# Performance work log

Measured on AMD Instinct MI355X. Metric: run time of the kernel, lower is better.

## Reference

```python
import jax, jax.numpy as jnp
import numpy as np

B, S, D, H, DK, DV, DFF, WIN = 2, 2048, 1024, 16, 64, 64, 4096, 128


def _layernorm(x, g, b, eps=1e-5):
    m = jnp.mean(x, axis=-1, keepdims=True)
    v = jnp.var(x, axis=-1, keepdims=True)
    return (x - m) / jnp.sqrt(v + eps) * g + b


def _attn_block(x, wq, bq, wk, bk, wv, bv, wo, bo, g, be, use_band):
    bsz, seq = x.shape[0], x.shape[1]
    q = (x @ wq + bq).reshape(bsz, seq, H, DK).transpose(0, 2, 1, 3)  # [B,H,S,DK]
    k = (x @ wk + bk).reshape(bsz, seq, H, DK).transpose(0, 2, 1, 3)
    v = (x @ wv + bv).reshape(bsz, seq, H, DV).transpose(0, 2, 1, 3)
    scores = jnp.einsum('bhqd,bhkd->bhqk', q, k) / np.sqrt(DK).astype(x.dtype)
    if use_band:
        i = jnp.arange(seq)
        band = jnp.abs(i[:, None] - i[None, :]) < WIN  # |i-j| < n_window
        scores = jnp.where(band[None, None], scores, -jnp.inf)
    attn = jax.nn.softmax(scores, axis=-1)
    ctx = jnp.einsum('bhqk,bhkd->bhqd', attn, v)  # [B,H,S,DV]
    ctx = ctx.transpose(0, 2, 1, 3).reshape(bsz, seq, H * DV)
    out = ctx @ wo + bo
    return _layernorm(out + x, g, be), attn


def _ffn(x, wc1, bc1, wc2, bc2, g, be):
    # conv1d with kernel_size=1 == pointwise linear
    h = jax.nn.relu(x @ wc1 + bc1)
    out = h @ wc2 + bc2
    return _layernorm(out + x, g, be)


def setup_inputs() -> dict:
    key = jax.random.key(0)
    ks = jax.random.split(key, 16)
    sc = 0.02
    inp = {'x': jax.random.normal(ks[0], (B, S, D), jnp.float32)}
    def lin(k, i, o):
        return jax.random.normal(k, (i, o), jnp.float32) * sc
    # full MHA params
    inp.update(wq1=lin(ks[1], D, H * DK), bq1=jnp.zeros((H * DK,)),
               wk1=lin(ks[2], D, H * DK), bk1=jnp.zeros((H * DK,)),
               wv1=lin(ks[3], D, H * DV), bv1=jnp.zeros((H * DV,)),
               wo1=lin(ks[4], H * DV, D), bo1=jnp.zeros((D,)),
               g1=jnp.ones((D,)), be1=jnp.zeros((D,)))
    # sliding-window attention params
    inp.update(wq2=lin(ks[5], D, H * DK), bq2=jnp.zeros((H * DK,)),
               wk2=lin(ks[6], D, H * DK), bk2=jnp.zeros((H * DK,)),
               wv2=lin(ks[7], D, H * DV), bv2=jnp.zeros((H * DV,)),
               wo2=lin(ks[8], H * DV, D), bo2=jnp.zeros((D,)),
               g2=jnp.ones((D,)), be2=jnp.zeros((D,)))
    # FFN params (conv1d k=1 -> linear)
    inp.update(wc1=lin(ks[9], D, DFF), bc1=jnp.zeros((DFF,)),
               wc2=lin(ks[10], DFF, D), bc2=jnp.zeros((D,)),
               g3=jnp.ones((D,)), be3=jnp.zeros((D,)))
    return inp


def reference(x, wq1, bq1, wk1, bk1, wv1, bv1, wo1, bo1, g1, be1,
              wq2, bq2, wk2, bk2, wv2, bv2, wo2, bo2, g2, be2,
              wc1, bc1, wc2, bc2, g3, be3):
    full_out, attn = _attn_block(x, wq1, bq1, wk1, bk1, wv1, bv1, wo1, bo1, g1, be1, use_band=False)
    sw_out, _ = _attn_block(x, wq2, bq2, wk2, bk2, wv2, bv2, wo2, bo2, g2, be2, use_band=True)
    enc = _ffn(full_out + sw_out, wc1, bc1, wc2, bc2, g3, be3)
    return enc, attn
```

## Files before the change

kernel.cpp:

```cpp
#include <hip/hip_runtime.h>
#include <hip/hip_bf16.h>

typedef __bf16 bf16_t;
typedef bf16_t bf16x8 __attribute__((ext_vector_type(8)));
typedef float floatx4 __attribute__((ext_vector_type(4)));

#define BBS 2
#define SEQ 2048
#define DIM 1024
#define NH 16
#define HD 64
#define DFF_ 4096
#define NT (BBS*SEQ)

template<bool AF32, bool BF32, bool BT, bool OUTF32, bool RELU, bool BIAS>
__global__ __launch_bounds__(256) void gemm64(
    const void* __restrict__ Av, const void* __restrict__ Bv,
    const float* __restrict__ bias, void* __restrict__ Cout,
    int M, int N, int K, int lda, int ldb, int ldc,
    int batchH, long long sAb, long long sAh, long long sBb, long long sBh,
    long long sCb, long long sCh, float scale)
{
    int z = blockIdx.z;
    int zb = z / batchH, zh = z - zb * batchH;
    long long aoff = zb * sAb + zh * sAh;
    long long boff = zb * sBb + zh * sBh;
    long long coff = zb * sCb + zh * sCh;
    const bf16_t* A16 = (const bf16_t*)Av + aoff;
    const float*  A32 = (const float*)Av + aoff;
    const bf16_t* B16 = (const bf16_t*)Bv + boff;
    const float*  B32 = (const float*)Bv + boff;

    int tile_n = blockIdx.x * 64;
    int tile_m = blockIdx.y * 64;

    __shared__ __align__(16) bf16_t Alds[64 * 72];
    __shared__ __align__(16) bf16_t Blds[64 * 72];

    int tid  = threadIdx.x;
    int wave = tid >> 6;
    int lane = tid & 63;
    int lm = lane & 15;
    int lq = lane >> 4;

    floatx4 acc[4];
    #pragma unroll
    for (int i = 0; i < 4; ++i) acc[i] = (floatx4){0.f, 0.f, 0.f, 0.f};

    int s_row  = tid >> 2;
    int s_koff = (tid & 3) * 16;
    int nb_k   = tid >> 3;
    int nb_noff= (tid & 7) * 8;

    int nkt = K >> 6;
    for (int kt = 0; kt < nkt; ++kt) {
        int k0 = kt << 6;
        if constexpr (AF32) {
            const float* src = A32 + (long long)(tile_m + s_row) * lda + (k0 + s_koff);
            float4 f0 = ((const float4*)src)[0];
            float4 f1 = ((const float4*)src)[1];
            float4 f2 = ((const float4*)src)[2];
            float4 f3 = ((const float4*)src)[3];
            bf16x8 h0, h1;
            h0[0]=(bf16_t)f0.x; h0[1]=(bf16_t)f0.y; h0[2]=(bf16_t)f0.z; h0[3]=(bf16_t)f0.w;
            h0[4]=(bf16_t)f1.x; h0[5]=(bf16_t)f1.y; h0[6]=(bf16_t)f1.z; h0[7]=(bf16_t)f1.w;
            h1[0]=(bf16_t)f2.x; h1[1]=(bf16_t)f2.y; h1[2]=(bf16_t)f2.z; h1[3]=(bf16_t)f2.w;
            h1[4]=(bf16_t)f3.x; h1[5]=(bf16_t)f3.y; h1[6]=(bf16_t)f3.z; h1[7]=(bf16_t)f3.w;
            *(bf16x8*)&Alds[s_row * 72 + s_koff]     = h0;
            *(bf16x8*)&Alds[s_row * 72 + s_koff + 8] = h1;
        } else {
            const bf16_t* src = A16 + (long long)(tile_m + s_row) * lda + (k0 + s_koff);
            *(uint4*)&Alds[s_row * 72 + s_koff]     = *(const uint4*)src;
            *(uint4*)&Alds[s_row * 72 + s_koff + 8] = *(const uint4*)(src + 8);
        }
        if constexpr (BT) {
            const bf16_t* src = B16 + (long long)(tile_n + s_row) * ldb + (k0 + s_koff);
            *(uint4*)&Blds[s_row * 72 + s_koff]     = *(const uint4*)src;
            *(uint4*)&Blds[s_row * 72 + s_koff + 8] = *(const uint4*)(src + 8);
        } else if constexpr (BF32) {
            #pragma unroll
            for (int kk = 0; kk < 64; kk += 32) {
                int k = kk + nb_k;
                const float* src = B32 + (long long)(k0 + k) * ldb + (tile_n + nb_noff);
                float4 f0 = ((const float4*)src)[0];
                float4 f1 = ((const float4*)src)[1];
                Blds[(nb_noff + 0) * 72 + k] = (bf16_t)f0.x;
                Blds[(nb_noff + 1) * 72 + k] = (bf16_t)f0.y;
                Blds[(nb_noff + 2) * 72 + k] = (bf16_t)f0.z;
                Blds[(nb_noff + 3) * 72 + k] = (bf16_t)f0.w;
                Blds[(nb_noff + 4) * 72 + k] = (bf16_t)f1.x;
                Blds[(nb_noff + 5) * 72 + k] = (bf16_t)f1.y;
                Blds[(nb_noff + 6) * 72 + k] = (bf16_t)f1.z;
                Blds[(nb_noff + 7) * 72 + k] = (bf16_t)f1.w;
            }
        } else {
            #pragma unroll
            for (int kk = 0; kk < 64; kk += 32) {
                int k = kk + nb_k;
                bf16x8 v = *(const bf16x8*)(B16 + (long long)(k0 + k) * ldb + (tile_n + nb_noff));
                #pragma unroll
                for (int j = 0; j < 8; ++j)
                    Blds[(nb_noff + j) * 72 + k] = v[j];
            }
        }
        __syncthreads();
        #pragma unroll
        for (int ks = 0; ks < 2; ++ks) {
            bf16x8 af = *(const bf16x8*)&Alds[(wave * 16 + lm) * 72 + ks * 32 + lq * 8];
            #pragma unroll
            for (int nt = 0; nt < 4; ++nt) {
                bf16x8 bfr = *(const bf16x8*)&Blds[(nt * 16 + lm) * 72 + ks * 32 + lq * 8];
                acc[nt] = __builtin_amdgcn_mfma_f32_16x16x32_bf16(af, bfr, acc[nt], 0, 0, 0);
            }
        }
        __syncthreads();
    }

    #pragma unroll
    for (int nt = 0; nt < 4; ++nt) {
        int col = tile_n + nt * 16 + lm;
        float bv = 0.f;
        if constexpr (BIAS) bv = bias[col];
        #pragma unroll
        for (int r = 0; r < 4; ++r) {
            int row = tile_m + wave * 16 + lq * 4 + r;
            float v = acc[nt][r] * scale + bv;
            if constexpr (RELU) v = fmaxf(v, 0.f);
            long long idx = coff + (long long)row * ldc + col;
            if constexpr (OUTF32) ((float*)Cout)[idx] = v;
            else                  ((bf16_t*)Cout)[idx] = (bf16_t)v;
        }
    }
}

__global__ __launch_bounds__(256) void softmax_f32(float* __restrict__ p)
{
    int row  = blockIdx.x * 4 + (threadIdx.x >> 6);
    int lane = threadIdx.x & 63;
    float* pr = p + (long long)row * SEQ;
    float v[32];
    float mx = -3.4e38f;
    #pragma unroll
    for (int it = 0; it < 8; ++it) {
        float4 c = *(const float4*)(pr + it * 256 + lane * 4);
        v[it*4+0] = c.x; v[it*4+1] = c.y; v[it*4+2] = c.z; v[it*4+3] = c.w;
        mx = fmaxf(mx, fmaxf(fmaxf(c.x, c.y), fmaxf(c.z, c.w)));
    }
    for (int off = 32; off; off >>= 1) mx = fmaxf(mx, __shfl_xor(mx, off));
    float s = 0.f;
    #pragma unroll
    for (int i = 0; i < 32; ++i) { v[i] = __expf(v[i] - mx); s += v[i]; }
    for (int off = 32; off; off >>= 1) s += __shfl_xor(s, off);
    float inv = 1.f / s;
    #pragma unroll
    for (int it = 0; it < 8; ++it) {
        float4 c;
        c.x = v[it*4+0]*inv; c.y = v[it*4+1]*inv; c.z = v[it*4+2]*inv; c.w = v[it*4+3]*inv;
        *(float4*)(pr + it * 256 + lane * 4) = c;
    }
}

__global__ __launch_bounds__(256) void sw_attn_mfma(
    const bf16_t* __restrict__ Q, const bf16_t* __restrict__ K,
    const bf16_t* __restrict__ V, bf16_t* __restrict__ ctx)
{
    int qt = blockIdx.x, h = blockIdx.y, b = blockIdx.z;
    int i0 = qt * 64;
    long long headoff = (long long)b * SEQ * DIM + (long long)h * HD;
    const bf16_t* Qb = Q + headoff;
    const bf16_t* Kb = K + headoff;
    const bf16_t* Vb = V + headoff;

    __shared__ __align__(16) bf16_t Klds[64 * 72];
    __shared__ __align__(16) bf16_t Vlds[64 * 72];
    __shared__ __align__(16) bf16_t Plds[64 * 72];

    int tid  = threadIdx.x;
    int wave = tid >> 6;
    int lane = tid & 63;
    int lm = lane & 15;
    int lq = lane >> 4;
    int s_row  = tid >> 2;
    int s_koff = (tid & 3) * 16;
    int nb_j   = tid >> 3;
    int nb_doff= (tid & 7) * 8;

    {
        const bf16_t* src = Qb + (long long)(i0 + s_row) * DIM + s_koff;
        *(uint4*)&Klds[s_row * 72 + s_koff]     = *(const uint4*)src;
        *(uint4*)&Klds[s_row * 72 + s_koff + 8] = *(const uint4*)(src + 8);
    }
    __syncthreads();
    bf16x8 qf0 = *(const bf16x8*)&Klds[(wave * 16 + lm) * 72 + 0 * 32 + lq * 8];
    bf16x8 qf1 = *(const bf16x8*)&Klds[(wave * 16 + lm) * 72 + 1 * 32 + lq * 8];
    __syncthreads();

    float m[4], l[4];
    floatx4 oacc[4];
    #pragma unroll
    for (int r = 0; r < 4; ++r) { m[r] = -1e30f; l[r] = 0.f; }
    #pragma unroll
    for (int nt = 0; nt < 4; ++nt) oacc[nt] = (floatx4){0.f, 0.f, 0.f, 0.f};

    int ibase = i0 + wave * 16 + lq * 4;

    for (int t = 0; t < 5; ++t) {
        int j0 = i0 - 128 + t * 64;
        if (j0 < 0 || j0 >= SEQ) continue;
        {
            const bf16_t* src = Kb + (long long)(j0 + s_row) * DIM + s_koff;
            *(uint4*)&Klds[s_row * 72 + s_koff]     = *(const uint4*)src;
            *(uint4*)&Klds[s_row * 72 + s_koff + 8] = *(const uint4*)(src + 8);
        }
        #pragma unroll
        for (int jj = 0; jj < 64; jj += 32) {
            int j = jj + nb_j;
            bf16x8 v = *(const bf16x8*)(Vb + (long long)(j0 + j) * DIM + nb_doff);
            #pragma unroll
            for (int e = 0; e < 8; ++e)
                Vlds[(nb_doff + e) * 72 + j] = v[e];
        }
        __syncthreads();

        floatx4 sacc[4];
        #pragma unroll
        for (int nt = 0; nt < 4; ++nt) sacc[nt] = (floatx4){0.f, 0.f, 0.f, 0.f};
        #pragma unroll
        for (int ks = 0; ks < 2; ++ks) {
            bf16x8 af = ks ? qf1 : qf0;
            #pragma unroll
            for (int nt = 0; nt < 4; ++nt) {
                bf16x8 bfr = *(const bf16x8*)&Klds[(nt * 16 + lm) * 72 + ks * 32 + lq * 8];
                sacc[nt] = __builtin_amdgcn_mfma_f32_16x16x32_bf16(af, bfr, sacc[nt], 0, 0, 0);
            }
        }

        float pmax[4] = {-3.4e38f, -3.4e38f, -3.4e38f, -3.4e38f};
        #pragma unroll
        for (int nt = 0; nt < 4; ++nt) {
            int j = j0 + nt * 16 + lm;
            #pragma unroll
            for (int r = 0; r < 4; ++r) {
                float s = sacc[nt][r] * 0.125f;
                int dd = ibase + r - j;
                if (dd > 127 || dd < -127) s = -3.0e38f;
                sacc[nt][r] = s;
                pmax[r] = fmaxf(pmax[r], s);
            }
        }
        #pragma unroll
        for (int off = 1; off < 16; off <<= 1) {
            #pragma unroll
            for (int r = 0; r < 4; ++r)
                pmax[r] = fmaxf(pmax[r], __shfl_xor(pmax[r], off));
        }
        float corr[4];
        #pragma unroll
        for (int r = 0; r < 4; ++r) {
            float mn = fmaxf(m[r], pmax[r]);
            corr[r] = __expf(m[r] - mn);
            m[r] = mn;
            l[r] *= corr[r];
        }
        float rs[4] = {0.f, 0.f, 0.f, 0.f};
        #pragma unroll
        for (int nt = 0; nt < 4; ++nt) {
            #pragma unroll
            for (int r = 0; r < 4; ++r) {
                float p = __expf(sacc[nt][r] - m[r]);
                sacc[nt][r] = p;
                rs[r] += p;
            }
        }
        #pragma unroll
        for (int off = 1; off < 16; off <<= 1) {
            #pragma unroll
            for (int r = 0; r < 4; ++r)
                rs[r] += __shfl_xor(rs[r], off);
        }
        #pragma unroll
        for (int r = 0; r < 4; ++r) l[r] += rs[r];

        #pragma unroll
        for (int nt = 0; nt < 4; ++nt) {
            #pragma unroll
            for (int r = 0; r < 4; ++r) {
                oacc[nt][r] *= corr[r];
                Plds[(wave * 16 + lq * 4 + r) * 72 + nt * 16 + lm] = (bf16_t)sacc[nt][r];
            }
        }

        #pragma unroll
        for (int ks = 0; ks < 2; ++ks) {
            bf16x8 af = *(const bf16x8*)&Plds[(wave * 16 + lm) * 72 + ks * 32 + lq * 8];
            #pragma unroll
            for (int nt = 0; nt < 4; ++nt) {
                bf16x8 bfr = *(const bf16x8*)&Vlds[(nt * 16 + lm) * 72 + ks * 32 + lq * 8];
                oacc[nt] = __builtin_amdgcn_mfma_f32_16x16x32_bf16(af, bfr, oacc[nt], 0, 0, 0);
            }
        }
        __syncthreads();
    }

    #pragma unroll
    for (int nt = 0; nt < 4; ++nt) {
        int d = nt * 16 + lm;
        #pragma unroll
        for (int r = 0; r < 4; ++r) {
            int i = ibase + r;
            ctx[(long long)(b * SEQ + i) * DIM + (long long)h * HD + d] =
                (bf16_t)(oacc[nt][r] / l[r]);
        }
    }
}

__global__ __launch_bounds__(256) void add_ln2_kernel(
    const float* __restrict__ o1, const float* __restrict__ o2,
    const float* __restrict__ x,
    const float* __restrict__ g1, const float* __restrict__ be1,
    const float* __restrict__ g2, const float* __restrict__ be2,
    bf16_t* __restrict__ sum_bf, float* __restrict__ sum_f)
{
    __shared__ float red[8];
    int t = blockIdx.x, tid = threadIdx.x;
    long long base = (long long)t * DIM;
    float a[4], b[4];
    float s1 = 0.f, s2 = 0.f;
    #pragma unroll
    for (int k = 0; k < 4; ++k) {
        int c = tid + k * 256;
        float xv = x[base + c];
        a[k] = o1[base + c] + xv;
        b[k] = o2[base + c] + xv;
        s1 += a[k]; s2 += b[k];
    }
    for (int off = 32; off; off >>= 1) { s1 += __shfl_xor(s1, off); s2 += __shfl_xor(s2, off); }
    if ((tid & 63) == 0) { red[tid >> 6] = s1; red[(tid >> 6) + 4] = s2; }
    __syncthreads();
    float m1 = (red[0] + red[1] + red[2] + red[3]) * (1.f / DIM);
    float m2 = (red[4] + red[5] + red[6] + red[7]) * (1.f / DIM);
    __syncthreads();
    float v1 = 0.f, v2 = 0.f;
    #pragma unroll
    for (int k = 0; k < 4; ++k) {
        float d1 = a[k] - m1, d2 = b[k] - m2;
        v1 += d1 * d1; v2 += d2 * d2;
    }
    for (int off = 32; off; off >>= 1) { v1 += __shfl_xor(v1, off); v2 += __shfl_xor(v2, off); }
    if ((tid & 63) == 0) { red[tid >> 6] = v1; red[(tid >> 6) + 4] = v2; }
    __syncthreads();
    v1 = (red[0] + red[1] + red[2] + red[3]) * (1.f / DIM);
    v2 = (red[4] + red[5] + red[6] + red[7]) * (1.f / DIM);
    float i1 = rsqrtf(v1 + 1e-5f), i2 = rsqrtf(v2 + 1e-5f);
    #pragma unroll
    for (int k = 0; k < 4; ++k) {
        int c = tid + k * 256;
        float va = (a[k] - m1) * i1 * g1[c] + be1[c];
        float vb = (b[k] - m2) * i2 * g2[c] + be2[c];
        float s  = va + vb;
        sum_f[base + c]  = s;
        sum_bf[base + c] = (bf16_t)s;
    }
}

__global__ __launch_bounds__(256) void final_ln_kernel(
    const float* __restrict__ ffn, const float* __restrict__ res,
    const float* __restrict__ g, const float* __restrict__ be,
    float* __restrict__ out)
{
    __shared__ float red[4];
    int t = blockIdx.x, tid = threadIdx.x;
    long long base = (long long)t * DIM;
    float a[4]; float s = 0.f;
    #pragma unroll
    for (int k = 0; k < 4; ++k) {
        int c = tid + k * 256;
        a[k] = ffn[base + c] + res[base + c];
        s += a[k];
    }
    for (int off = 32; off; off >>= 1) s += __shfl_xor(s, off);
    if ((tid & 63) == 0) red[tid >> 6] = s;
    __syncthreads();
    float m = (red[0] + red[1] + red[2] + red[3]) * (1.f / DIM);
    __syncthreads();
    float v = 0.f;
    #pragma unroll
    for (int k = 0; k < 4; ++k) { float d = a[k] - m; v += d * d; }
    for (int off = 32; off; off >>= 1) v += __shfl_xor(v, off);
    if ((tid & 63) == 0) red[tid >> 6] = v;
    __syncthreads();
    v = (red[0] + red[1] + red[2] + red[3]) * (1.f / DIM);
    float inv = rsqrtf(v + 1e-5f);
    #pragma unroll
    for (int k = 0; k < 4; ++k) {
        int c = tid + k * 256;
        out[base + c] = (a[k] - m) * inv * g[c] + be[c];
    }
}

extern "C" void kernel_launch(void* const* d_in, const int* in_sizes, int n_in,
                              void* d_out, int out_size, void* d_ws, size_t ws_size,
                              hipStream_t stream)
{
    const float* x   = (const float*)d_in[0];
    const float* wq1 = (const float*)d_in[1];
    const float* bq1 = (const float*)d_in[2];
    const float* wk1 = (const float*)d_in[3];
    const float* bk1 = (const float*)d_in[4];
    const float* wv1 = (const float*)d_in[5];
    const float* bv1 = (const float*)d_in[6];
    const float* wo1 = (const float*)d_in[7];
    const float* bo1 = (const float*)d_in[8];
    const float* g1  = (const float*)d_in[9];
    const float* be1 = (const float*)d_in[10];
    const float* wq2 = (const float*)d_in[11];
    const float* bq2 = (const float*)d_in[12];
    const float* wk2 = (const float*)d_in[13];
    const float* bk2 = (const float*)d_in[14];
    const float* wv2 = (const float*)d_in[15];
    const float* bv2 = (const float*)d_in[16];
    const float* wo2 = (const float*)d_in[17];
    const float* bo2 = (const float*)d_in[18];
    const float* g2  = (const float*)d_in[19];
    const float* be2 = (const float*)d_in[20];
    const float* wc1 = (const float*)d_in[21];
    const float* bc1 = (const float*)d_in[22];
    const float* wc2 = (const float*)d_in[23];
    const float* bc2 = (const float*)d_in[24];
    const float* g3  = (const float*)d_in[25];
    const float* be3 = (const float*)d_in[26];

    float* enc_out  = (float*)d_out;
    float* attn_out = enc_out + (long long)NT * DIM;

    const size_t NTD = (size_t)NT * DIM;
    bf16_t* qb = (bf16_t*)d_ws;
    bf16_t* kb = qb + NTD;
    bf16_t* vb = kb + NTD;
    bf16_t* cb = vb + NTD;
    float*  o1 = (float*)(cb + NTD);
    float*  o2 = o1 + NTD;
    bf16_t* sumbf = (bf16_t*)(o2 + NTD);
    float*  sumf  = (float*)(sumbf + NTD);
    bf16_t* hbuf = qb;
    float*  ffo  = o1;

    dim3 blk(256);
    const long long SD = (long long)SEQ * DIM;
    const long long SS = (long long)SEQ * SEQ;

    gemm64<true,true,false,false,false,true><<<dim3(16,64,1),blk,0,stream>>>(x, wq2, bq2, qb, NT,DIM,DIM, DIM,DIM,DIM, 1, 0,0,0,0,0,0, 1.f);
    gemm64<true,true,false,false,false,true><<<dim3(16,64,1),blk,0,stream>>>(x, wk2, bk2, kb, NT,DIM,DIM, DIM,DIM,DIM, 1, 0,0,0,0,0,0, 1.f);
    gemm64<true,true,false,false,false,true><<<dim3(16,64,1),blk,0,stream>>>(x, wv2, bv2, vb, NT,DIM,DIM, DIM,DIM,DIM, 1, 0,0,0,0,0,0, 1.f);
    sw_attn_mfma<<<dim3(SEQ/64, NH, BBS),blk,0,stream>>>(qb, kb, vb, cb);
    gemm64<false,true,false,true,false,true><<<dim3(16,64,1),blk,0,stream>>>(cb, wo2, bo2, o2, NT,DIM,DIM, DIM,DIM,DIM, 1, 0,0,0,0,0,0, 1.f);

    gemm64<true,true,false,false,false,true><<<dim3(16,64,1),blk,0,stream>>>(x, wq1, bq1, qb, NT,DIM,DIM, DIM,DIM,DIM, 1, 0,0,0,0,0,0, 1.f);
    gemm64<true,true,false,false,false,true><<<dim3(16,64,1),blk,0,stream>>>(x, wk1, bk1, kb, NT,DIM,DIM, DIM,DIM,DIM, 1, 0,0,0,0,0,0, 1.f);
    gemm64<true,true,false,false,false,true><<<dim3(16,64,1),blk,0,stream>>>(x, wv1, bv1, vb, NT,DIM,DIM, DIM,DIM,DIM, 1, 0,0,0,0,0,0, 1.f);

    gemm64<false,false,true,true,false,false><<<dim3(32,32,32),blk,0,stream>>>(
        qb, kb, nullptr, attn_out, SEQ,SEQ,HD, DIM,DIM,SEQ,
        NH, SD,(long long)HD, SD,(long long)HD, (long long)NH*SS, SS, 0.125f);

    softmax_f32<<<dim3((BBS*NH*SEQ)/4),blk,0,stream>>>(attn_out);

    gemm64<true,false,false,false,false,false><<<dim3(1,32,32),blk,0,stream>>>(
        attn_out, vb, nullptr, cb, SEQ,HD,SEQ, SEQ,DIM,DIM,
        NH, (long long)NH*SS, SS, SD,(long long)HD, SD,(long long)HD, 1.f);

    gemm64<false,true,false,true,false,true><<<dim3(16,64,1),blk,0,stream>>>(cb, wo1, bo1, o1, NT,DIM,DIM, DIM,DIM,DIM, 1, 0,0,0,0,0,0, 1.f);

    add_ln2_kernel<<<dim3(NT),blk,0,stream>>>(o1, o2, x, g1, be1, g2, be2, sumbf, sumf);

    gemm64<false,true,false,false,true,true><<<dim3(64,64,1),blk,0,stream>>>(sumbf, wc1, bc1, hbuf, NT,DFF_,DIM, DIM,DFF_,DFF_, 1, 0,0,0,0,0,0, 1.f);
    gemm64<false,true,false,true,false,true><<<dim3(16,64,1),blk,0,stream>>>(hbuf, wc2, bc2, ffo, NT,DIM,DFF_, DFF_,DIM,DIM, 1, 0,0,0,0,0,0, 1.f);

    final_ln_kernel<<<dim3(NT),blk,0,stream>>>(ffo, sumf, g3, be3, enc_out);
}
```

Baseline: 1.823 ms.

## Fuse full attention QK^T, softmax and PV into one two-pass kernel

Replaces the batched score GEMM, the in-place fp32 softmax and the probability-times-V GEMM with one kernel per 64-query tile. A first pass over all keys computes the row max and normalizer online; a second pass recomputes the scores, writes the normalized probabilities once, and accumulates the context with MFMA from a bf16 copy held in shared memory. This cuts the repeated reads and writes of the large fp32 attention matrix, at the cost of computing QK^T twice and a transposed V store with scalar LDS writes.

```diff
diff --git a/kernel.cpp b/kernel.cpp
--- a/kernel.cpp
+++ b/kernel.cpp
@@ -133,30 +133,182 @@
     }
 }
 
-__global__ __launch_bounds__(256) void softmax_f32(float* __restrict__ p)
+__global__ __launch_bounds__(256) void full_attn_fused(
+    const bf16_t* __restrict__ Q, const bf16_t* __restrict__ K,
+    const bf16_t* __restrict__ V, float* __restrict__ probs,
+    bf16_t* __restrict__ ctx)
 {
-    int row  = blockIdx.x * 4 + (threadIdx.x >> 6);
-    int lane = threadIdx.x & 63;
-    float* pr = p + (long long)row * SEQ;
-    float v[32];
-    float mx = -3.4e38f;
-    #pragma unroll
-    for (int it = 0; it < 8; ++it) {
-        float4 c = *(const float4*)(pr + it * 256 + lane * 4);
-        v[it*4+0] = c.x; v[it*4+1] = c.y; v[it*4+2] = c.z; v[it*4+3] = c.w;
-        mx = fmaxf(mx, fmaxf(fmaxf(c.x, c.y), fmaxf(c.z, c.w)));
-    }
-    for (int off = 32; off; off >>= 1) mx = fmaxf(mx, __shfl_xor(mx, off));
-    float s = 0.f;
-    #pragma unroll
-    for (int i = 0; i < 32; ++i) { v[i] = __expf(v[i] - mx); s += v[i]; }
-    for (int off = 32; off; off >>= 1) s += __shfl_xor(s, off);
-    float inv = 1.f / s;
-    #pragma unroll
-    for (int it = 0; it < 8; ++it) {
-        float4 c;
-        c.x = v[it*4+0]*inv; c.y = v[it*4+1]*inv; c.z = v[it*4+2]*inv; c.w = v[it*4+3]*inv;
-        *(float4*)(pr + it * 256 + lane * 4) = c;
+    int qt = blockIdx.x, h = blockIdx.y, b = blockIdx.z;
+    int i0 = qt * 64;
+    long long headoff = (long long)b * SEQ * DIM + (long long)h * HD;
+    const bf16_t* Qb = Q + headoff;
+    const bf16_t* Kb = K + headoff;
+    const bf16_t* Vb = V + headoff;
+    float* Pb = probs + ((long long)(b * NH + h)) * SEQ * SEQ;
+
+    __shared__ __align__(16) bf16_t Klds[64 * 72];
+    __shared__ __align__(16) bf16_t Vlds[64 * 72];
+    __shared__ __align__(16) bf16_t Plds[64 * 72];
+
+    int tid  = threadIdx.x;
+    int wave = tid >> 6;
+    int lane = tid & 63;
+    int lm = lane & 15;
+    int lq = lane >> 4;
+    int s_row  = tid >> 2;
+    int s_koff = (tid & 3) * 16;
+    int nb_j   = tid >> 3;
+    int nb_doff= (tid & 7) * 8;
+
+    {
+        const bf16_t* src = Qb + (long long)(i0 + s_row) * DIM + s_koff;
+        *(uint4*)&Klds[s_row * 72 + s_koff]     = *(const uint4*)src;
+        *(uint4*)&Klds[s_row * 72 + s_koff + 8] = *(const uint4*)(src + 8);
+    }
+    __syncthreads();
+    bf16x8 qf0 = *(const bf16x8*)&Klds[(wave * 16 + lm) * 72 + 0 * 32 + lq * 8];
+    bf16x8 qf1 = *(const bf16x8*)&Klds[(wave * 16 + lm) * 72 + 1 * 32 + lq * 8];
+    __syncthreads();
+
+    float m[4], l[4];
+    #pragma unroll
+    for (int r = 0; r < 4; ++r) { m[r] = -3.4e38f; l[r] = 0.f; }
+
+    for (int tt = 0; tt < SEQ / 128; ++tt) {
+        int j0 = tt * 128;
+        {
+            const bf16_t* src = Kb + (long long)(j0 + s_row) * DIM + s_koff;
+            *(uint4*)&Klds[s_row * 72 + s_koff]     = *(const uint4*)src;
+            *(uint4*)&Klds[s_row * 72 + s_koff + 8] = *(const uint4*)(src + 8);
+            const bf16_t* src2 = src + (long long)64 * DIM;
+            *(uint4*)&Vlds[s_row * 72 + s_koff]     = *(const uint4*)src2;
+            *(uint4*)&Vlds[s_row * 72 + s_koff + 8] = *(const uint4*)(src2 + 8);
+        }
+        __syncthreads();
+
+        floatx4 s0[4], s1[4];
+        #pragma unroll
+        for (int nt = 0; nt < 4; ++nt) { s0[nt] = (floatx4){0,0,0,0}; s1[nt] = (floatx4){0,0,0,0}; }
+        #pragma unroll
+        for (int ks = 0; ks < 2; ++ks) {
+            bf16x8 af = ks ? qf1 : qf0;
+            #pragma unroll
+            for (int nt = 0; nt < 4; ++nt) {
+                bf16x8 b0 = *(const bf16x8*)&Klds[(nt * 16 + lm) * 72 + ks * 32 + lq * 8];
+                s0[nt] = __builtin_amdgcn_mfma_f32_16x16x32_bf16(af, b0, s0[nt], 0, 0, 0);
+                bf16x8 b1 = *(const bf16x8*)&Vlds[(nt * 16 + lm) * 72 + ks * 32 + lq * 8];
+                s1[nt] = __builtin_amdgcn_mfma_f32_16x16x32_bf16(af, b1, s1[nt], 0, 0, 0);
+            }
+        }
+        float pmax[4] = {-3.4e38f, -3.4e38f, -3.4e38f, -3.4e38f};
+        #pragma unroll
+        for (int nt = 0; nt < 4; ++nt) {
+            #pragma unroll
+            for (int r = 0; r < 4; ++r) {
+                float a = s0[nt][r] * 0.125f, c = s1[nt][r] * 0.125f;
+                s0[nt][r] = a; s1[nt][r] = c;
+                pmax[r] = fmaxf(pmax[r], fmaxf(a, c));
+            }
+        }
+        #pragma unroll
+        for (int off = 1; off < 16; off <<= 1) {
+            #pragma unroll
+            for (int r = 0; r < 4; ++r)
+                pmax[r] = fmaxf(pmax[r], __shfl_xor(pmax[r], off));
+        }
+        float rs[4] = {0.f, 0.f, 0.f, 0.f};
+        #pragma unroll
+        for (int r = 0; r < 4; ++r) {
+            float mn = fmaxf(m[r], pmax[r]);
+            l[r] *= __expf(m[r] - mn);
+            m[r] = mn;
+        }
+        #pragma unroll
+        for (int nt = 0; nt < 4; ++nt) {
+            #pragma unroll
+            for (int r = 0; r < 4; ++r)
+                rs[r] += __expf(s0[nt][r] - m[r]) + __expf(s1[nt][r] - m[r]);
+        }
+        #pragma unroll
+        for (int off = 1; off < 16; off <<= 1) {
+            #pragma unroll
+            for (int r = 0; r < 4; ++r)
+                rs[r] += __shfl_xor(rs[r], off);
+        }
+        #pragma unroll
+        for (int r = 0; r < 4; ++r) l[r] += rs[r];
+        __syncthreads();
+    }
+
+    float invl[4];
+    #pragma unroll
+    for (int r = 0; r < 4; ++r) invl[r] = 1.f / l[r];
+
+    floatx4 oacc[4];
+    #pragma unroll
+    for (int nt = 0; nt < 4; ++nt) oacc[nt] = (floatx4){0.f, 0.f, 0.f, 0.f};
+
+    int irow = wave * 16 + lq * 4;
+
+    for (int t = 0; t < SEQ / 64; ++t) {
+        int j0 = t * 64;
+        {
+            const bf16_t* src = Kb + (long long)(j0 + s_row) * DIM + s_koff;
+            *(uint4*)&Klds[s_row * 72 + s_koff]     = *(const uint4*)src;
+            *(uint4*)&Klds[s_row * 72 + s_koff + 8] = *(const uint4*)(src + 8);
+        }
+        #pragma unroll
+        for (int jj = 0; jj < 64; jj += 32) {
+            int j = jj + nb_j;
+            bf16x8 v = *(const bf16x8*)(Vb + (long long)(j0 + j) * DIM + nb_doff);
+            #pragma unroll
+            for (int e = 0; e < 8; ++e)
+                Vlds[(nb_doff + e) * 72 + j] = v[e];
+        }
+        __syncthreads();
+
+        floatx4 sacc[4];
+        #pragma unroll
+        for (int nt = 0; nt < 4; ++nt) sacc[nt] = (floatx4){0,0,0,0};
+        #pragma unroll
+        for (int ks = 0; ks < 2; ++ks) {
+            bf16x8 af = ks ? qf1 : qf0;
+            #pragma unroll
+            for (int nt = 0; nt < 4; ++nt) {
+                bf16x8 bfr = *(const bf16x8*)&Klds[(nt * 16 + lm) * 72 + ks * 32 + lq * 8];
+                sacc[nt] = __builtin_amdgcn_mfma_f32_16x16x32_bf16(af, bfr, sacc[nt], 0, 0, 0);
+            }
+        }
+        #pragma unroll
+        for (int nt = 0; nt < 4; ++nt) {
+            int col = j0 + nt * 16 + lm;
+            #pragma unroll
+            for (int r = 0; r < 4; ++r) {
+                float p = __expf(sacc[nt][r] * 0.125f - m[r]) * invl[r];
+                Pb[(long long)(i0 + irow + r) * SEQ + col] = p;
+                Plds[(irow + r) * 72 + nt * 16 + lm] = (bf16_t)p;
+            }
+        }
+        #pragma unroll
+        for (int ks = 0; ks < 2; ++ks) {
+            bf16x8 af = *(const bf16x8*)&Plds[(wave * 16 + lm) * 72 + ks * 32 + lq * 8];
+            #pragma unroll
+            for (int nt = 0; nt < 4; ++nt) {
+                bf16x8 bfr = *(const bf16x8*)&Vlds[(nt * 16 + lm) * 72 + ks * 32 + lq * 8];
+                oacc[nt] = __builtin_amdgcn_mfma_f32_16x16x32_bf16(af, bfr, oacc[nt], 0, 0, 0);
+            }
+        }
+        __syncthreads();
+    }
+
+    #pragma unroll
+    for (int nt = 0; nt < 4; ++nt) {
+        int d = nt * 16 + lm;
+        #pragma unroll
+        for (int r = 0; r < 4; ++r) {
+            int i = i0 + irow + r;
+            ctx[(long long)(b * SEQ + i) * DIM + (long long)h * HD + d] = (bf16_t)oacc[nt][r];
+        }
     }
 }
 
@@ -446,8 +598,6 @@
     float*  ffo  = o1;
 
     dim3 blk(256);
-    const long long SD = (long long)SEQ * DIM;
-    const long long SS = (long long)SEQ * SEQ;
 
     gemm64<true,true,false,false,false,true><<<dim3(16,64,1),blk,0,stream>>>(x, wq2, bq2, qb, NT,DIM,DIM, DIM,DIM,DIM, 1, 0,0,0,0,0,0, 1.f);
     gemm64<true,true,false,false,false,true><<<dim3(16,64,1),blk,0,stream>>>(x, wk2, bk2, kb, NT,DIM,DIM, DIM,DIM,DIM, 1, 0,0,0,0,0,0, 1.f);
@@ -459,15 +609,7 @@
     gemm64<true,true,false,false,false,true><<<dim3(16,64,1),blk,0,stream>>>(x, wk1, bk1, kb, NT,DIM,DIM, DIM,DIM,DIM, 1, 0,0,0,0,0,0, 1.f);
     gemm64<true,true,false,false,false,true><<<dim3(16,64,1),blk,0,stream>>>(x, wv1, bv1, vb, NT,DIM,DIM, DIM,DIM,DIM, 1, 0,0,0,0,0,0, 1.f);
 
-    gemm64<false,false,true,true,false,false><<<dim3(32,32,32),blk,0,stream>>>(
-        qb, kb, nullptr, attn_out, SEQ,SEQ,HD, DIM,DIM,SEQ,
-        NH, SD,(long long)HD, SD,(long long)HD, (long long)NH*SS, SS, 0.125f);
-
-    softmax_f32<<<dim3((BBS*NH*SEQ)/4),blk,0,stream>>>(attn_out);
-
-    gemm64<true,false,false,false,false,false><<<dim3(1,32,32),blk,0,stream>>>(
-        attn_out, vb, nullptr, cb, SEQ,HD,SEQ, SEQ,DIM,DIM,
-        NH, (long long)NH*SS, SS, SD,(long long)HD, SD,(long long)HD, 1.f);
+    full_attn_fused<<<dim3(SEQ/64, NH, BBS),blk,0,stream>>>(qb, kb, vb, attn_out, cb);
 
     gemm64<false,true,false,true,false,true><<<dim3(16,64,1),blk,0,stream>>>(cb, wo1, bo1, o1, NT,DIM,DIM, DIM,DIM,DIM, 1, 0,0,0,0,0,0, 1.f);
 
```

New measurement: 1.604 ms. 12.0% less time.
